# Kernel tuning notes

Measured on AMD Instinct MI355X. Metric: run time of the kernel, lower is better.

## Reference

```python
import jax, jax.numpy as jnp
import numpy as np

N, F, H, T, E, HOR = 50000, 24, 128, 12, 800000, 6


def setup_inputs() -> dict:
    key = jax.random.key(0)
    ks = jax.random.split(key, 16)
    x_seq = jax.random.normal(ks[0], (T, N, F), jnp.float32)
    ei_seq = jax.random.randint(ks[1], (T, 2, E), 0, N, jnp.int32)
    ea_seq = jax.random.uniform(ks[2], (T, E), jnp.float32)
    mask_seq = jax.random.bernoulli(ks[3], 0.9, (T, N))
    s = 1.0 / float(np.sqrt(H))
    def w(k, shape):
        return jax.random.uniform(k, shape, jnp.float32, -s, s)
    params = dict(
        Wz=w(ks[4], (F, H)), Wr=w(ks[5], (F, H)), Wh=w(ks[6], (F, H)),
        bz=jnp.zeros((H,), jnp.float32), br=jnp.zeros((H,), jnp.float32), bh=jnp.zeros((H,), jnp.float32),
        LWz=w(ks[7], (2 * H, H)), LWr=w(ks[8], (2 * H, H)), LWh=w(ks[9], (2 * H, H)),
        Lbz=w(ks[10], (H,)), Lbr=w(ks[11], (H,)), Lbh=w(ks[12], (H,)),
        headW=w(ks[13], (H, F)), headb=w(ks[14], (F,)),
    )
    return dict(x_seq=x_seq, ei_seq=ei_seq, ea_seq=ea_seq, mask_seq=mask_seq, id_seq=0, **params)


def _gcn(x, src, dst, ew, W, b):
    xw = x @ W                                                     # [N,H]
    deg = jnp.zeros((x.shape[0],), xw.dtype).at[dst].add(ew) + 1.0  # in-degree + self-loop
    dinv = jax.lax.rsqrt(deg)
    coef = dinv[src] * ew * dinv[dst]                              # [E]
    agg = jnp.zeros_like(xw).at[dst].add(xw[src] * coef[:, None])
    return agg + xw * (1.0 / deg)[:, None] + b                     # normalized self-loop term


def _cell(x, src, dst, ew, h, p):
    # TGCN (GCN-GRU) cell from pytorch_geometric_temporal
    z = jax.nn.sigmoid(jnp.concatenate([_gcn(x, src, dst, ew, p['Wz'], p['bz']), h], 1) @ p['LWz'] + p['Lbz'])
    r = jax.nn.sigmoid(jnp.concatenate([_gcn(x, src, dst, ew, p['Wr'], p['br']), h], 1) @ p['LWr'] + p['Lbr'])
    htil = jnp.tanh(jnp.concatenate([_gcn(x, src, dst, ew, p['Wh'], p['bh']), h * r], 1) @ p['LWh'] + p['Lbh'])
    return z * h + (1.0 - z) * htil


def _forward(x_seq, ei_seq, ea_seq, mask_seq, p):
    Nn, Hh = x_seq.shape[1], p['LWz'].shape[1]

    # Encoder over T steps: h_store keeps last hidden of every node ever present
    def enc(carry, inp):
        h_store, seen = carry
        x, ei, ew, mask = inp
        h_prev = jnp.where((mask & seen)[:, None], h_store, 0.0)
        h_new = _cell(x, ei[0], ei[1], ew, h_prev, p)
        return (jnp.where(mask[:, None], h_new, h_store), seen | mask), None

    init = (jnp.zeros((Nn, Hh), x_seq.dtype), jnp.zeros((Nn,), bool))
    (h_store, seen), _ = jax.lax.scan(enc, init, (x_seq, ei_seq, ea_seq, mask_seq))

    h_prev = jnp.where((mask_seq[-1] & seen)[:, None], h_store, 0.0)
    src_l, dst_l, ew_l = ei_seq[-1, 0], ei_seq[-1, 1], ea_seq[-1]

    def dec(carry, _):
        h, inp = carry
        h_new = _cell(inp, src_l, dst_l, ew_l, h, p)
        y = h_new @ p['headW'] + p['headb']
        return (h_new, y), y

    _, preds = jax.lax.scan(dec, (h_prev, x_seq[-1]), None, length=HOR)
    return preds  # [horizon, N, out_channels]


def reference(x_seq, ei_seq, ea_seq, mask_seq, id_seq, Wz, Wr, Wh, bz, br, bh,
              LWz, LWr, LWh, Lbz, Lbr, Lbh, headW, headb):
    p = dict(Wz=Wz, Wr=Wr, Wh=Wh, bz=bz, br=br, bh=bh,
             LWz=LWz, LWr=LWr, LWh=LWh, Lbz=Lbz, Lbr=Lbr, Lbh=Lbh,
             headW=headW, headb=headb)
    return _forward(x_seq, ei_seq, ea_seq, mask_seq, p)
```

## Files before the change

kernel.cpp:

```cpp
#include <hip/hip_runtime.h>

#define NN 50000
#define FF 24
#define HH 128
#define TT 12
#define EE 800000
#define HORZ 6


__global__ void k_maskdetect(const unsigned char* __restrict__ m, int* __restrict__ flag) {
    int i = blockIdx.x * 256 + threadIdx.x;
    if (i < 16384 && (i & 3) != 0 && m[i] != 0) atomicOr(flag, 1);
}

__global__ void k_maskconv(const unsigned char* __restrict__ mraw, const int* __restrict__ flag,
                           unsigned char* __restrict__ mout) {
    int i = blockIdx.x * 256 + threadIdx.x;
    if (i >= TT * NN) return;
    if (*flag) mout[i] = (mraw[i] != 0);
    else       mout[i] = (((const int*)mraw)[i] != 0);
}


__global__ void k_hist(const int* __restrict__ ei, int* __restrict__ cnt) {
    int idx = blockIdx.x * 256 + threadIdx.x;
    if (idx >= TT * EE) return;
    int t = idx / EE, e = idx - t * EE;
    int dst = ei[((size_t)t * 2 + 1) * EE + e];
    atomicAdd(&cnt[t * NN + dst], 1);
}

__global__ void k_scan(const int* __restrict__ cnt, int* __restrict__ offs,
                       int* __restrict__ cursor) {
    __shared__ int sums[1024];
    int t = blockIdx.x, tid = threadIdx.x;
    const int per = (NN + 1023) / 1024;
    int base = tid * per;
    int s = 0;
    for (int i = 0; i < per; i++) {
        int idx = base + i;
        if (idx < NN) s += cnt[t * NN + idx];
    }
    sums[tid] = s;
    __syncthreads();
    for (int off = 1; off < 1024; off <<= 1) {
        int tv = (tid >= off) ? sums[tid - off] : 0;
        __syncthreads();
        sums[tid] += tv;
        __syncthreads();
    }
    int run = sums[tid] - s;
    for (int i = 0; i < per; i++) {
        int idx = base + i;
        if (idx < NN) {
            offs[t * (NN + 1) + idx] = run;
            cursor[t * NN + idx] = run;
            run += cnt[t * NN + idx];
        }
    }
    if (tid == 1023) offs[t * (NN + 1) + NN] = sums[1023];
}

__global__ void k_fill(const int* __restrict__ ei, const float* __restrict__ ea,
                       int* __restrict__ cursor, int* __restrict__ srcs,
                       float* __restrict__ eav) {
    int idx = blockIdx.x * 256 + threadIdx.x;
    if (idx >= TT * EE) return;
    int t = idx / EE, e = idx - t * EE;
    int dst = ei[((size_t)t * 2 + 1) * EE + e];
    int src = ei[((size_t)t * 2 + 0) * EE + e];
    int pos = atomicAdd(&cursor[t * NN + dst], 1);
    srcs[(size_t)t * EE + pos] = src;
    eav[(size_t)t * EE + pos]  = ea[(size_t)t * EE + e];
}

__global__ void k_degdinv(const int* __restrict__ offs, const float* __restrict__ eav,
                          float* __restrict__ dinv) {
    int idx = blockIdx.x * 256 + threadIdx.x;
    if (idx >= TT * NN) return;
    int t = idx / NN, n = idx - t * NN;
    int b = offs[t * (NN + 1) + n], en = offs[t * (NN + 1) + n + 1];
    float s = 0.f;
    for (int j = b; j < en; j++) s += eav[(size_t)t * EE + j];
    dinv[idx] = rsqrtf(s + 1.0f);
}

__global__ void k_coef(const int* __restrict__ offs, const int* __restrict__ srcs,
                       const float* __restrict__ dinv, float* __restrict__ eav) {
    int idx = blockIdx.x * 256 + threadIdx.x;
    if (idx >= TT * NN) return;
    int t = idx / NN, n = idx - t * NN;
    int b = offs[t * (NN + 1) + n], en = offs[t * (NN + 1) + n + 1];
    float di = dinv[idx];
    for (int j = b; j < en; j++) {
        int s = srcs[(size_t)t * EE + j];
        eav[(size_t)t * EE + j] *= di * dinv[t * NN + s];
    }
}


__global__ void k_fold(const float* __restrict__ Wz, const float* __restrict__ Wr,
                       const float* __restrict__ Wh,
                       const float* __restrict__ bz, const float* __restrict__ br,
                       const float* __restrict__ bh,
                       const float* __restrict__ LWz, const float* __restrict__ LWr,
                       const float* __restrict__ LWh,
                       const float* __restrict__ Lbz, const float* __restrict__ Lbr,
                       const float* __restrict__ Lbh,
                       float* __restrict__ Call, float* __restrict__ b2) {
    int g = blockIdx.x, c = threadIdx.x;
    const float* W  = g == 0 ? Wz : (g == 1 ? Wr : Wh);
    const float* LW = g == 0 ? LWz : (g == 1 ? LWr : LWh);
    const float* bg = g == 0 ? bz : (g == 1 ? br : bh);
    const float* Lb = g == 0 ? Lbz : (g == 1 ? Lbr : Lbh);
    for (int j = 0; j < FF; j++) {
        float a = 0.f;
        for (int k = 0; k < HH; k++) a += W[j * HH + k] * LW[k * HH + c];
        Call[((size_t)g * FF + j) * HH + c] = a;
    }
    float a = Lb[c];
    for (int k = 0; k < HH; k++) a += bg[k] * LW[k * HH + c];
    b2[g * HH + c] = a;
}


__global__ void k_gather(const float* __restrict__ x, const int* __restrict__ offs,
                         const int* __restrict__ srcs, const float* __restrict__ eav,
                         const float* __restrict__ dinv, float* __restrict__ xe) {
    int idx = blockIdx.x * 256 + threadIdx.x;
    if (idx >= NN * FF) return;
    int n = idx / FF, f = idx - n * FF;
    int b = offs[n], en = offs[n + 1];
    float di = dinv[n];
    float acc = x[idx] * di * di;
    for (int j = b; j < en; j++) {
        acc += x[srcs[j] * FF + f] * eav[j];
    }
    xe[idx] = acc;
}


#define FMA8X(SARR, M0, K)                                                        \
    {                                                                             \
        float4 v_;                                                                \
        v_ = *(const float4*)&SARR[M0 + 0][K]; a0 += v_.x*w0 + v_.y*w1 + v_.z*w2 + v_.w*w3; \
        v_ = *(const float4*)&SARR[M0 + 1][K]; a1 += v_.x*w0 + v_.y*w1 + v_.z*w2 + v_.w*w3; \
        v_ = *(const float4*)&SARR[M0 + 2][K]; a2 += v_.x*w0 + v_.y*w1 + v_.z*w2 + v_.w*w3; \
        v_ = *(const float4*)&SARR[M0 + 3][K]; a3 += v_.x*w0 + v_.y*w1 + v_.z*w2 + v_.w*w3; \
        v_ = *(const float4*)&SARR[M0 + 4][K]; a4 += v_.x*w0 + v_.y*w1 + v_.z*w2 + v_.w*w3; \
        v_ = *(const float4*)&SARR[M0 + 5][K]; a5 += v_.x*w0 + v_.y*w1 + v_.z*w2 + v_.w*w3; \
        v_ = *(const float4*)&SARR[M0 + 6][K]; a6 += v_.x*w0 + v_.y*w1 + v_.z*w2 + v_.w*w3; \
        v_ = *(const float4*)&SARR[M0 + 7][K]; a7 += v_.x*w0 + v_.y*w1 + v_.z*w2 + v_.w*w3; \
    }

template <int DOHEAD>
__global__ __launch_bounds__(256) void k_cell(
        const float* __restrict__ xe, const float* __restrict__ hin,
        const unsigned char* __restrict__ gmask,
        const float* __restrict__ Call, const float* __restrict__ b2,
        const float* __restrict__ LWz, const float* __restrict__ LWr,
        const float* __restrict__ LWh,
        const unsigned char* __restrict__ wmask, float* __restrict__ hout,
        const float* __restrict__ headW, const float* __restrict__ headb,
        float* __restrict__ y) {
    __shared__ float s_xe[16][FF];
    __shared__ float s_h0[16][HH];
    __shared__ float s_z[16][HH];
    __shared__ float s_hr[16][HH];
    int nb = blockIdx.x * 16;
    int tid = threadIdx.x;

    for (int i = tid; i < 16 * FF; i += 256) {
        s_xe[i / FF][i % FF] = xe[(size_t)nb * FF + i];
    }
    for (int i = tid; i < 16 * HH; i += 256) {
        int m = i >> 7, k = i & 127;
        float v = hin[((size_t)nb + m) * HH + k];
        if (gmask && !gmask[nb + m]) v = 0.f;
        s_h0[m][k] = v;
    }
    __syncthreads();

    int g = tid >> 7, c = tid & 127;

    {
        const float* Cg   = Call + (size_t)g * FF * HH;
        const float* LWgb = (g ? LWr : LWz) + (size_t)HH * HH;
        float bb = b2[g * HH + c];
#pragma unroll
        for (int ch = 0; ch < 2; ch++) {
            int m0 = ch * 8;
            float a0 = bb, a1 = bb, a2 = bb, a3 = bb, a4 = bb, a5 = bb, a6 = bb, a7 = bb;
#pragma unroll
            for (int k = 0; k < FF; k += 4) {
                float w0 = Cg[(k + 0) * HH + c], w1 = Cg[(k + 1) * HH + c];
                float w2 = Cg[(k + 2) * HH + c], w3 = Cg[(k + 3) * HH + c];
                FMA8X(s_xe, m0, k);
            }
#pragma unroll 4
            for (int k = 0; k < HH; k += 4) {
                float w0 = LWgb[(k + 0) * HH + c], w1 = LWgb[(k + 1) * HH + c];
                float w2 = LWgb[(k + 2) * HH + c], w3 = LWgb[(k + 3) * HH + c];
                FMA8X(s_h0, m0, k);
            }
#pragma unroll
            for (int r = 0; r < 8; r++) {
                float a = (r == 0) ? a0 : (r == 1) ? a1 : (r == 2) ? a2 : (r == 3) ? a3
                        : (r == 4) ? a4 : (r == 5) ? a5 : (r == 6) ? a6 : a7;
                float s = 1.f / (1.f + __expf(-a));
                if (g == 0) s_z[m0 + r][c] = s;
                else        s_hr[m0 + r][c] = s * s_h0[m0 + r][c];
            }
        }
    }
    __syncthreads();

    {
        const float* Ch   = Call + (size_t)2 * FF * HH;
        const float* LWhb = LWh + (size_t)HH * HH;
        float bb = b2[2 * HH + c];
        int m0 = g * 8;
        float a0 = bb, a1 = bb, a2 = bb, a3 = bb, a4 = bb, a5 = bb, a6 = bb, a7 = bb;
#pragma unroll
        for (int k = 0; k < FF; k += 4) {
            float w0 = Ch[(k + 0) * HH + c], w1 = Ch[(k + 1) * HH + c];
            float w2 = Ch[(k + 2) * HH + c], w3 = Ch[(k + 3) * HH + c];
            FMA8X(s_xe, m0, k);
        }
#pragma unroll 4
        for (int k = 0; k < HH; k += 4) {
            float w0 = LWhb[(k + 0) * HH + c], w1 = LWhb[(k + 1) * HH + c];
            float w2 = LWhb[(k + 2) * HH + c], w3 = LWhb[(k + 3) * HH + c];
            FMA8X(s_hr, m0, k);
        }
#pragma unroll
        for (int r = 0; r < 8; r++) {
            float a = (r == 0) ? a0 : (r == 1) ? a1 : (r == 2) ? a2 : (r == 3) ? a3
                    : (r == 4) ? a4 : (r == 5) ? a5 : (r == 6) ? a6 : a7;
            int m = m0 + r;
            float e2 = __expf(2.f * a);
            float ht = 1.f - 2.f / (e2 + 1.f);
            float z = s_z[m][c];
            float h0v = s_h0[m][c];
            float hn = z * h0v + (1.f - z) * ht;
            int n = nb + m;
            if (wmask) {
                if (wmask[n]) hout[(size_t)n * HH + c] = hn;
            } else {
                hout[(size_t)n * HH + c] = hn;
            }
            if (DOHEAD) s_z[m][c] = hn;
        }
    }

    if (DOHEAD) {
        __syncthreads();
        for (int i = tid; i < 16 * FF; i += 256) {
            int m = i / FF, f = i - m * FF;
            float acc = headb[f];
#pragma unroll 8
            for (int cJ = 0; cJ < HH; cJ++) acc += s_z[m][cJ] * headW[cJ * FF + f];
            y[(size_t)nb * FF + i] = acc;
        }
    }
}

extern "C" void kernel_launch(void* const* d_in, const int* in_sizes, int n_in,
                              void* d_out, int out_size, void* d_ws, size_t ws_size,
                              hipStream_t stream) {
    const float* x_seq = (const float*)d_in[0];
    const int*   ei    = (const int*)d_in[1];
    const float* ea    = (const float*)d_in[2];
    const unsigned char* mraw = (const unsigned char*)d_in[3];
    const float* Wz  = (const float*)d_in[5];
    const float* Wr  = (const float*)d_in[6];
    const float* Wh  = (const float*)d_in[7];
    const float* bz  = (const float*)d_in[8];
    const float* br  = (const float*)d_in[9];
    const float* bh  = (const float*)d_in[10];
    const float* LWz = (const float*)d_in[11];
    const float* LWr = (const float*)d_in[12];
    const float* LWh = (const float*)d_in[13];
    const float* Lbz = (const float*)d_in[14];
    const float* Lbr = (const float*)d_in[15];
    const float* Lbh = (const float*)d_in[16];
    const float* headW = (const float*)d_in[17];
    const float* headb = (const float*)d_in[18];
    float* out = (float*)d_out;

    char* wp = (char*)d_ws;
    int*   cnt    = (int*)wp;   wp += sizeof(int) * TT * NN;
    int*   cursor = (int*)wp;   wp += sizeof(int) * TT * NN;
    int*   offs   = (int*)wp;   wp += sizeof(int) * TT * (NN + 1);
    int*   srcs   = (int*)wp;   wp += sizeof(int) * (size_t)TT * EE;
    float* eav    = (float*)wp; wp += sizeof(float) * (size_t)TT * EE;
    float* dinv   = (float*)wp; wp += sizeof(float) * TT * NN;
    float* hstore = (float*)wp; wp += sizeof(float) * (size_t)NN * HH;
    float* hp     = (float*)wp; wp += sizeof(float) * (size_t)NN * HH;
    float* xebuf  = (float*)wp; wp += sizeof(float) * NN * FF;
    float* Call   = (float*)wp; wp += sizeof(float) * 3 * FF * HH;
    float* b2     = (float*)wp; wp += sizeof(float) * 3 * HH;
    int*   mflag  = (int*)wp;   wp += 256;
    unsigned char* mask = (unsigned char*)wp; wp += TT * NN;
    if (ws_size < (size_t)(wp - (char*)d_ws)) return;

    hipMemsetAsync(mflag, 0, sizeof(int), stream);
    k_maskdetect<<<64, 256, 0, stream>>>(mraw, mflag);
    k_maskconv<<<(TT * NN + 255) / 256, 256, 0, stream>>>(mraw, mflag, mask);

    hipMemsetAsync(cnt, 0, sizeof(int) * TT * NN, stream);
    hipMemsetAsync(hstore, 0, sizeof(float) * NN * HH, stream);
    k_hist<<<(TT * EE + 255) / 256, 256, 0, stream>>>(ei, cnt);
    k_scan<<<TT, 1024, 0, stream>>>(cnt, offs, cursor);
    k_fill<<<(TT * EE + 255) / 256, 256, 0, stream>>>(ei, ea, cursor, srcs, eav);
    k_degdinv<<<(TT * NN + 255) / 256, 256, 0, stream>>>(offs, eav, dinv);
    k_coef<<<(TT * NN + 255) / 256, 256, 0, stream>>>(offs, srcs, dinv, eav);
    k_fold<<<3, 128, 0, stream>>>(Wz, Wr, Wh, bz, br, bh, LWz, LWr, LWh, Lbz, Lbr, Lbh, Call, b2);

    for (int t = 0; t < TT; t++) {
        const float* xt = x_seq + (size_t)t * NN * FF;
        const unsigned char* mt = mask + (size_t)t * NN;
        k_gather<<<(NN * FF + 255) / 256, 256, 0, stream>>>(
            xt, offs + t * (NN + 1), srcs + (size_t)t * EE, eav + (size_t)t * EE,
            dinv + t * NN, xebuf);
        k_cell<0><<<NN / 16, 256, 0, stream>>>(
            xebuf, hstore, mt, Call, b2, LWz, LWr, LWh, mt, hstore,
            nullptr, nullptr, nullptr);
    }

    const int*   offsl = offs + (TT - 1) * (NN + 1);
    const int*   srcsl = srcs + (size_t)(TT - 1) * EE;
    const float* eavl  = eav + (size_t)(TT - 1) * EE;
    const float* dil   = dinv + (TT - 1) * NN;
    for (int k = 0; k < HORZ; k++) {
        const float* xin = (k == 0) ? (x_seq + (size_t)(TT - 1) * NN * FF)
                                    : (out + (size_t)(k - 1) * NN * FF);
        k_gather<<<(NN * FF + 255) / 256, 256, 0, stream>>>(
            xin, offsl, srcsl, eavl, dil, xebuf);
        k_cell<1><<<NN / 16, 256, 0, stream>>>(
            xebuf, (k == 0) ? hstore : hp,
            (k == 0) ? (mask + (size_t)(TT - 1) * NN) : nullptr,
            Call, b2, LWz, LWr, LWh, nullptr, hp,
            headW, headb, out + (size_t)k * NN * FF);
    }
}
```

Before: 5.121 ms.

## Pack CSR edges into int2 and compute z and r gates together per thread

```diff
diff --git a/kernel.cpp b/kernel.cpp
--- a/kernel.cpp
+++ b/kernel.cpp
@@ -62,39 +62,38 @@
 }
 
 __global__ void k_fill(const int* __restrict__ ei, const float* __restrict__ ea,
-                       int* __restrict__ cursor, int* __restrict__ srcs,
-                       float* __restrict__ eav) {
+                       int* __restrict__ cursor, int2* __restrict__ edges) {
     int idx = blockIdx.x * 256 + threadIdx.x;
     if (idx >= TT * EE) return;
     int t = idx / EE, e = idx - t * EE;
     int dst = ei[((size_t)t * 2 + 1) * EE + e];
     int src = ei[((size_t)t * 2 + 0) * EE + e];
     int pos = atomicAdd(&cursor[t * NN + dst], 1);
-    srcs[(size_t)t * EE + pos] = src;
-    eav[(size_t)t * EE + pos]  = ea[(size_t)t * EE + e];
-}
-
-__global__ void k_degdinv(const int* __restrict__ offs, const float* __restrict__ eav,
+    edges[(size_t)t * EE + pos] = make_int2(src, __float_as_int(ea[(size_t)t * EE + e]));
+}
+
+__global__ void k_degdinv(const int* __restrict__ offs, const int2* __restrict__ edges,
                           float* __restrict__ dinv) {
     int idx = blockIdx.x * 256 + threadIdx.x;
     if (idx >= TT * NN) return;
     int t = idx / NN, n = idx - t * NN;
     int b = offs[t * (NN + 1) + n], en = offs[t * (NN + 1) + n + 1];
     float s = 0.f;
-    for (int j = b; j < en; j++) s += eav[(size_t)t * EE + j];
+    for (int j = b; j < en; j++) s += __int_as_float(edges[(size_t)t * EE + j].y);
     dinv[idx] = rsqrtf(s + 1.0f);
 }
 
-__global__ void k_coef(const int* __restrict__ offs, const int* __restrict__ srcs,
-                       const float* __restrict__ dinv, float* __restrict__ eav) {
+__global__ void k_coef(const int* __restrict__ offs, const float* __restrict__ dinv,
+                       int2* __restrict__ edges) {
     int idx = blockIdx.x * 256 + threadIdx.x;
     if (idx >= TT * NN) return;
     int t = idx / NN, n = idx - t * NN;
     int b = offs[t * (NN + 1) + n], en = offs[t * (NN + 1) + n + 1];
     float di = dinv[idx];
     for (int j = b; j < en; j++) {
-        int s = srcs[(size_t)t * EE + j];
-        eav[(size_t)t * EE + j] *= di * dinv[t * NN + s];
+        int2 p = edges[(size_t)t * EE + j];
+        float v = __int_as_float(p.y) * di * dinv[t * NN + p.x];
+        edges[(size_t)t * EE + j].y = __float_as_int(v);
     }
 }
 
@@ -125,7 +124,7 @@
 
 
 __global__ void k_gather(const float* __restrict__ x, const int* __restrict__ offs,
-                         const int* __restrict__ srcs, const float* __restrict__ eav,
+                         const int2* __restrict__ edges,
                          const float* __restrict__ dinv, float* __restrict__ xe) {
     int idx = blockIdx.x * 256 + threadIdx.x;
     if (idx >= NN * FF) return;
@@ -134,11 +133,41 @@
     float di = dinv[n];
     float acc = x[idx] * di * di;
     for (int j = b; j < en; j++) {
-        acc += x[srcs[j] * FF + f] * eav[j];
+        int2 p = edges[j];
+        acc += x[p.x * FF + f] * __int_as_float(p.y);
     }
     xe[idx] = acc;
 }
 
+
+#define FMA8X2(SARR, M0, K)                                                                  \
+    {                                                                                        \
+        float4 v_;                                                                           \
+        v_ = *(const float4*)&SARR[M0 + 0][K];                                               \
+        az0 += v_.x*wz0 + v_.y*wz1 + v_.z*wz2 + v_.w*wz3;                                    \
+        ar0 += v_.x*wr0 + v_.y*wr1 + v_.z*wr2 + v_.w*wr3;                                    \
+        v_ = *(const float4*)&SARR[M0 + 1][K];                                               \
+        az1 += v_.x*wz0 + v_.y*wz1 + v_.z*wz2 + v_.w*wz3;                                    \
+        ar1 += v_.x*wr0 + v_.y*wr1 + v_.z*wr2 + v_.w*wr3;                                    \
+        v_ = *(const float4*)&SARR[M0 + 2][K];                                               \
+        az2 += v_.x*wz0 + v_.y*wz1 + v_.z*wz2 + v_.w*wz3;                                    \
+        ar2 += v_.x*wr0 + v_.y*wr1 + v_.z*wr2 + v_.w*wr3;                                    \
+        v_ = *(const float4*)&SARR[M0 + 3][K];                                               \
+        az3 += v_.x*wz0 + v_.y*wz1 + v_.z*wz2 + v_.w*wz3;                                    \
+        ar3 += v_.x*wr0 + v_.y*wr1 + v_.z*wr2 + v_.w*wr3;                                    \
+        v_ = *(const float4*)&SARR[M0 + 4][K];                                               \
+        az4 += v_.x*wz0 + v_.y*wz1 + v_.z*wz2 + v_.w*wz3;                                    \
+        ar4 += v_.x*wr0 + v_.y*wr1 + v_.z*wr2 + v_.w*wr3;                                    \
+        v_ = *(const float4*)&SARR[M0 + 5][K];                                               \
+        az5 += v_.x*wz0 + v_.y*wz1 + v_.z*wz2 + v_.w*wz3;                                    \
+        ar5 += v_.x*wr0 + v_.y*wr1 + v_.z*wr2 + v_.w*wr3;                                    \
+        v_ = *(const float4*)&SARR[M0 + 6][K];                                               \
+        az6 += v_.x*wz0 + v_.y*wz1 + v_.z*wz2 + v_.w*wz3;                                    \
+        ar6 += v_.x*wr0 + v_.y*wr1 + v_.z*wr2 + v_.w*wr3;                                    \
+        v_ = *(const float4*)&SARR[M0 + 7][K];                                               \
+        az7 += v_.x*wz0 + v_.y*wz1 + v_.z*wz2 + v_.w*wz3;                                    \
+        ar7 += v_.x*wr0 + v_.y*wr1 + v_.z*wr2 + v_.w*wr3;                                    \
+    }
 
 #define FMA8X(SARR, M0, K)                                                        \
     {                                                                             \
@@ -182,35 +211,40 @@
     __syncthreads();
 
     int g = tid >> 7, c = tid & 127;
+    int m0 = g * 8;
 
     {
-        const float* Cg   = Call + (size_t)g * FF * HH;
-        const float* LWgb = (g ? LWr : LWz) + (size_t)HH * HH;
-        float bb = b2[g * HH + c];
+        const float* Cz   = Call;
+        const float* Cr   = Call + (size_t)FF * HH;
+        const float* LWzb = LWz + (size_t)HH * HH;
+        const float* LWrb = LWr + (size_t)HH * HH;
+        float bbz = b2[c], bbr = b2[HH + c];
+        float az0 = bbz, az1 = bbz, az2 = bbz, az3 = bbz, az4 = bbz, az5 = bbz, az6 = bbz, az7 = bbz;
+        float ar0 = bbr, ar1 = bbr, ar2 = bbr, ar3 = bbr, ar4 = bbr, ar5 = bbr, ar6 = bbr, ar7 = bbr;
 #pragma unroll
-        for (int ch = 0; ch < 2; ch++) {
-            int m0 = ch * 8;
-            float a0 = bb, a1 = bb, a2 = bb, a3 = bb, a4 = bb, a5 = bb, a6 = bb, a7 = bb;
+        for (int k = 0; k < FF; k += 4) {
+            float wz0 = Cz[(k + 0) * HH + c], wz1 = Cz[(k + 1) * HH + c];
+            float wz2 = Cz[(k + 2) * HH + c], wz3 = Cz[(k + 3) * HH + c];
+            float wr0 = Cr[(k + 0) * HH + c], wr1 = Cr[(k + 1) * HH + c];
+            float wr2 = Cr[(k + 2) * HH + c], wr3 = Cr[(k + 3) * HH + c];
+            FMA8X2(s_xe, m0, k);
+        }
+#pragma unroll 4
+        for (int k = 0; k < HH; k += 4) {
+            float wz0 = LWzb[(k + 0) * HH + c], wz1 = LWzb[(k + 1) * HH + c];
+            float wz2 = LWzb[(k + 2) * HH + c], wz3 = LWzb[(k + 3) * HH + c];
+            float wr0 = LWrb[(k + 0) * HH + c], wr1 = LWrb[(k + 1) * HH + c];
+            float wr2 = LWrb[(k + 2) * HH + c], wr3 = LWrb[(k + 3) * HH + c];
+            FMA8X2(s_h0, m0, k);
+        }
 #pragma unroll
-            for (int k = 0; k < FF; k += 4) {
-                float w0 = Cg[(k + 0) * HH + c], w1 = Cg[(k + 1) * HH + c];
-                float w2 = Cg[(k + 2) * HH + c], w3 = Cg[(k + 3) * HH + c];
-                FMA8X(s_xe, m0, k);
-            }
-#pragma unroll 4
-            for (int k = 0; k < HH; k += 4) {
-                float w0 = LWgb[(k + 0) * HH + c], w1 = LWgb[(k + 1) * HH + c];
-                float w2 = LWgb[(k + 2) * HH + c], w3 = LWgb[(k + 3) * HH + c];
-                FMA8X(s_h0, m0, k);
-            }
-#pragma unroll
-            for (int r = 0; r < 8; r++) {
-                float a = (r == 0) ? a0 : (r == 1) ? a1 : (r == 2) ? a2 : (r == 3) ? a3
-                        : (r == 4) ? a4 : (r == 5) ? a5 : (r == 6) ? a6 : a7;
-                float s = 1.f / (1.f + __expf(-a));
-                if (g == 0) s_z[m0 + r][c] = s;
-                else        s_hr[m0 + r][c] = s * s_h0[m0 + r][c];
-            }
+        for (int r = 0; r < 8; r++) {
+            float az = (r == 0) ? az0 : (r == 1) ? az1 : (r == 2) ? az2 : (r == 3) ? az3
+                     : (r == 4) ? az4 : (r == 5) ? az5 : (r == 6) ? az6 : az7;
+            float ar = (r == 0) ? ar0 : (r == 1) ? ar1 : (r == 2) ? ar2 : (r == 3) ? ar3
+                     : (r == 4) ? ar4 : (r == 5) ? ar5 : (r == 6) ? ar6 : ar7;
+            s_z[m0 + r][c]  = 1.f / (1.f + __expf(-az));
+            s_hr[m0 + r][c] = (1.f / (1.f + __expf(-ar))) * s_h0[m0 + r][c];
         }
     }
     __syncthreads();
@@ -219,7 +253,6 @@
         const float* Ch   = Call + (size_t)2 * FF * HH;
         const float* LWhb = LWh + (size_t)HH * HH;
         float bb = b2[2 * HH + c];
-        int m0 = g * 8;
         float a0 = bb, a1 = bb, a2 = bb, a3 = bb, a4 = bb, a5 = bb, a6 = bb, a7 = bb;
 #pragma unroll
         for (int k = 0; k < FF; k += 4) {
@@ -292,8 +325,7 @@
     int*   cnt    = (int*)wp;   wp += sizeof(int) * TT * NN;
     int*   cursor = (int*)wp;   wp += sizeof(int) * TT * NN;
     int*   offs   = (int*)wp;   wp += sizeof(int) * TT * (NN + 1);
-    int*   srcs   = (int*)wp;   wp += sizeof(int) * (size_t)TT * EE;
-    float* eav    = (float*)wp; wp += sizeof(float) * (size_t)TT * EE;
+    int2*  edges  = (int2*)wp;  wp += sizeof(int2) * (size_t)TT * EE;
     float* dinv   = (float*)wp; wp += sizeof(float) * TT * NN;
     float* hstore = (float*)wp; wp += sizeof(float) * (size_t)NN * HH;
     float* hp     = (float*)wp; wp += sizeof(float) * (size_t)NN * HH;
@@ -312,31 +344,29 @@
     hipMemsetAsync(hstore, 0, sizeof(float) * NN * HH, stream);
     k_hist<<<(TT * EE + 255) / 256, 256, 0, stream>>>(ei, cnt);
     k_scan<<<TT, 1024, 0, stream>>>(cnt, offs, cursor);
-    k_fill<<<(TT * EE + 255) / 256, 256, 0, stream>>>(ei, ea, cursor, srcs, eav);
-    k_degdinv<<<(TT * NN + 255) / 256, 256, 0, stream>>>(offs, eav, dinv);
-    k_coef<<<(TT * NN + 255) / 256, 256, 0, stream>>>(offs, srcs, dinv, eav);
+    k_fill<<<(TT * EE + 255) / 256, 256, 0, stream>>>(ei, ea, cursor, edges);
+    k_degdinv<<<(TT * NN + 255) / 256, 256, 0, stream>>>(offs, edges, dinv);
+    k_coef<<<(TT * NN + 255) / 256, 256, 0, stream>>>(offs, dinv, edges);
     k_fold<<<3, 128, 0, stream>>>(Wz, Wr, Wh, bz, br, bh, LWz, LWr, LWh, Lbz, Lbr, Lbh, Call, b2);
 
     for (int t = 0; t < TT; t++) {
         const float* xt = x_seq + (size_t)t * NN * FF;
         const unsigned char* mt = mask + (size_t)t * NN;
         k_gather<<<(NN * FF + 255) / 256, 256, 0, stream>>>(
-            xt, offs + t * (NN + 1), srcs + (size_t)t * EE, eav + (size_t)t * EE,
-            dinv + t * NN, xebuf);
+            xt, offs + t * (NN + 1), edges + (size_t)t * EE, dinv + t * NN, xebuf);
         k_cell<0><<<NN / 16, 256, 0, stream>>>(
             xebuf, hstore, mt, Call, b2, LWz, LWr, LWh, mt, hstore,
             nullptr, nullptr, nullptr);
     }
 
-    const int*   offsl = offs + (TT - 1) * (NN + 1);
-    const int*   srcsl = srcs + (size_t)(TT - 1) * EE;
-    const float* eavl  = eav + (size_t)(TT - 1) * EE;
+    const int*  offsl  = offs + (TT - 1) * (NN + 1);
+    const int2* edgesl = edges + (size_t)(TT - 1) * EE;
     const float* dil   = dinv + (TT - 1) * NN;
     for (int k = 0; k < HORZ; k++) {
         const float* xin = (k == 0) ? (x_seq + (size_t)(TT - 1) * NN * FF)
                                     : (out + (size_t)(k - 1) * NN * FF);
         k_gather<<<(NN * FF + 255) / 256, 256, 0, stream>>>(
-            xin, offsl, srcsl, eavl, dil, xebuf);
+            xin, offsl, edgesl, dil, xebuf);
         k_cell<1><<<NN / 16, 256, 0, stream>>>(
             xebuf, (k == 0) ? hstore : hp,
             (k == 0) ? (mask + (size_t)(TT - 1) * NN) : nullptr,
```

Result: no change. 5.121 ms (+0.0%).

## Fuse neighbor gather into GRU cell kernel and transpose weights for vector loads

Applied to the files above, without the earlier changes.

```diff
diff --git a/kernel.cpp b/kernel.cpp
--- a/kernel.cpp
+++ b/kernel.cpp
@@ -107,7 +107,9 @@
                        const float* __restrict__ LWh,
                        const float* __restrict__ Lbz, const float* __restrict__ Lbr,
                        const float* __restrict__ Lbh,
-                       float* __restrict__ Call, float* __restrict__ b2) {
+                       const float* __restrict__ headW,
+                       float* __restrict__ CallT, float* __restrict__ b2,
+                       float* __restrict__ LWT, float* __restrict__ headWT) {
     int g = blockIdx.x, c = threadIdx.x;
     const float* W  = g == 0 ? Wz : (g == 1 ? Wr : Wh);
     const float* LW = g == 0 ? LWz : (g == 1 ? LWr : LWh);
@@ -116,52 +118,75 @@
     for (int j = 0; j < FF; j++) {
         float a = 0.f;
         for (int k = 0; k < HH; k++) a += W[j * HH + k] * LW[k * HH + c];
-        Call[((size_t)g * FF + j) * HH + c] = a;
+        CallT[((size_t)g * HH + c) * FF + j] = a;
     }
     float a = Lb[c];
     for (int k = 0; k < HH; k++) a += bg[k] * LW[k * HH + c];
     b2[g * HH + c] = a;
-}
-
-
-__global__ void k_gather(const float* __restrict__ x, const int* __restrict__ offs,
-                         const int* __restrict__ srcs, const float* __restrict__ eav,
-                         const float* __restrict__ dinv, float* __restrict__ xe) {
-    int idx = blockIdx.x * 256 + threadIdx.x;
-    if (idx >= NN * FF) return;
-    int n = idx / FF, f = idx - n * FF;
-    int b = offs[n], en = offs[n + 1];
-    float di = dinv[n];
-    float acc = x[idx] * di * di;
-    for (int j = b; j < en; j++) {
-        acc += x[srcs[j] * FF + f] * eav[j];
-    }
-    xe[idx] = acc;
-}
-
-
-#define FMA8X(SARR, M0, K)                                                        \
-    {                                                                             \
-        float4 v_;                                                                \
-        v_ = *(const float4*)&SARR[M0 + 0][K]; a0 += v_.x*w0 + v_.y*w1 + v_.z*w2 + v_.w*w3; \
-        v_ = *(const float4*)&SARR[M0 + 1][K]; a1 += v_.x*w0 + v_.y*w1 + v_.z*w2 + v_.w*w3; \
-        v_ = *(const float4*)&SARR[M0 + 2][K]; a2 += v_.x*w0 + v_.y*w1 + v_.z*w2 + v_.w*w3; \
-        v_ = *(const float4*)&SARR[M0 + 3][K]; a3 += v_.x*w0 + v_.y*w1 + v_.z*w2 + v_.w*w3; \
-        v_ = *(const float4*)&SARR[M0 + 4][K]; a4 += v_.x*w0 + v_.y*w1 + v_.z*w2 + v_.w*w3; \
-        v_ = *(const float4*)&SARR[M0 + 5][K]; a5 += v_.x*w0 + v_.y*w1 + v_.z*w2 + v_.w*w3; \
-        v_ = *(const float4*)&SARR[M0 + 6][K]; a6 += v_.x*w0 + v_.y*w1 + v_.z*w2 + v_.w*w3; \
-        v_ = *(const float4*)&SARR[M0 + 7][K]; a7 += v_.x*w0 + v_.y*w1 + v_.z*w2 + v_.w*w3; \
+    for (int k = 0; k < HH; k++) {
+        LWT[((size_t)g * HH + c) * HH + k] = LW[(HH + k) * HH + c];
+    }
+    if (g == 0) {
+        for (int idx = c; idx < FF * HH; idx += 128) {
+            int f = idx / HH, cJ = idx - f * HH;
+            headWT[f * HH + cJ] = headW[cJ * FF + f];
+        }
+    }
+}
+
+
+#define FMA8X2(SARR, M0, K, WZ, WR)                                                          \
+    {                                                                                        \
+        float4 v_;                                                                           \
+        v_ = *(const float4*)&SARR[M0 + 0][K];                                               \
+        az0 += v_.x*WZ.x + v_.y*WZ.y + v_.z*WZ.z + v_.w*WZ.w;                                \
+        ar0 += v_.x*WR.x + v_.y*WR.y + v_.z*WR.z + v_.w*WR.w;                                \
+        v_ = *(const float4*)&SARR[M0 + 1][K];                                               \
+        az1 += v_.x*WZ.x + v_.y*WZ.y + v_.z*WZ.z + v_.w*WZ.w;                                \
+        ar1 += v_.x*WR.x + v_.y*WR.y + v_.z*WR.z + v_.w*WR.w;                                \
+        v_ = *(const float4*)&SARR[M0 + 2][K];                                               \
+        az2 += v_.x*WZ.x + v_.y*WZ.y + v_.z*WZ.z + v_.w*WZ.w;                                \
+        ar2 += v_.x*WR.x + v_.y*WR.y + v_.z*WR.z + v_.w*WR.w;                                \
+        v_ = *(const float4*)&SARR[M0 + 3][K];                                               \
+        az3 += v_.x*WZ.x + v_.y*WZ.y + v_.z*WZ.z + v_.w*WZ.w;                                \
+        ar3 += v_.x*WR.x + v_.y*WR.y + v_.z*WR.z + v_.w*WR.w;                                \
+        v_ = *(const float4*)&SARR[M0 + 4][K];                                               \
+        az4 += v_.x*WZ.x + v_.y*WZ.y + v_.z*WZ.z + v_.w*WZ.w;                                \
+        ar4 += v_.x*WR.x + v_.y*WR.y + v_.z*WR.z + v_.w*WR.w;                                \
+        v_ = *(const float4*)&SARR[M0 + 5][K];                                               \
+        az5 += v_.x*WZ.x + v_.y*WZ.y + v_.z*WZ.z + v_.w*WZ.w;                                \
+        ar5 += v_.x*WR.x + v_.y*WR.y + v_.z*WR.z + v_.w*WR.w;                                \
+        v_ = *(const float4*)&SARR[M0 + 6][K];                                               \
+        az6 += v_.x*WZ.x + v_.y*WZ.y + v_.z*WZ.z + v_.w*WZ.w;                                \
+        ar6 += v_.x*WR.x + v_.y*WR.y + v_.z*WR.z + v_.w*WR.w;                                \
+        v_ = *(const float4*)&SARR[M0 + 7][K];                                               \
+        az7 += v_.x*WZ.x + v_.y*WZ.y + v_.z*WZ.z + v_.w*WZ.w;                                \
+        ar7 += v_.x*WR.x + v_.y*WR.y + v_.z*WR.z + v_.w*WR.w;                                \
+    }
+
+#define FMA8X(SARR, M0, K, W4)                                                               \
+    {                                                                                        \
+        float4 v_;                                                                           \
+        v_ = *(const float4*)&SARR[M0 + 0][K]; a0 += v_.x*W4.x + v_.y*W4.y + v_.z*W4.z + v_.w*W4.w; \
+        v_ = *(const float4*)&SARR[M0 + 1][K]; a1 += v_.x*W4.x + v_.y*W4.y + v_.z*W4.z + v_.w*W4.w; \
+        v_ = *(const float4*)&SARR[M0 + 2][K]; a2 += v_.x*W4.x + v_.y*W4.y + v_.z*W4.z + v_.w*W4.w; \
+        v_ = *(const float4*)&SARR[M0 + 3][K]; a3 += v_.x*W4.x + v_.y*W4.y + v_.z*W4.z + v_.w*W4.w; \
+        v_ = *(const float4*)&SARR[M0 + 4][K]; a4 += v_.x*W4.x + v_.y*W4.y + v_.z*W4.z + v_.w*W4.w; \
+        v_ = *(const float4*)&SARR[M0 + 5][K]; a5 += v_.x*W4.x + v_.y*W4.y + v_.z*W4.z + v_.w*W4.w; \
+        v_ = *(const float4*)&SARR[M0 + 6][K]; a6 += v_.x*W4.x + v_.y*W4.y + v_.z*W4.z + v_.w*W4.w; \
+        v_ = *(const float4*)&SARR[M0 + 7][K]; a7 += v_.x*W4.x + v_.y*W4.y + v_.z*W4.z + v_.w*W4.w; \
     }
 
 template <int DOHEAD>
 __global__ __launch_bounds__(256) void k_cell(
-        const float* __restrict__ xe, const float* __restrict__ hin,
-        const unsigned char* __restrict__ gmask,
-        const float* __restrict__ Call, const float* __restrict__ b2,
-        const float* __restrict__ LWz, const float* __restrict__ LWr,
-        const float* __restrict__ LWh,
+        const float* __restrict__ x, const int* __restrict__ offs,
+        const int* __restrict__ srcs, const float* __restrict__ eav,
+        const float* __restrict__ dinv,
+        const float* __restrict__ hin, const unsigned char* __restrict__ gmask,
+        const float* __restrict__ CallT, const float* __restrict__ b2,
+        const float* __restrict__ LWT,
         const unsigned char* __restrict__ wmask, float* __restrict__ hout,
-        const float* __restrict__ headW, const float* __restrict__ headb,
+        const float* __restrict__ headWT, const float* __restrict__ headb,
         float* __restrict__ y) {
     __shared__ float s_xe[16][FF];
     __shared__ float s_h0[16][HH];
@@ -171,7 +196,15 @@
     int tid = threadIdx.x;
 
     for (int i = tid; i < 16 * FF; i += 256) {
-        s_xe[i / FF][i % FF] = xe[(size_t)nb * FF + i];
+        int m = i / FF, f = i - m * FF;
+        int n = nb + m;
+        int b = offs[n], en = offs[n + 1];
+        float di = dinv[n];
+        float acc = x[(size_t)n * FF + f] * di * di;
+        for (int j = b; j < en; j++) {
+            acc += x[(size_t)srcs[j] * FF + f] * eav[j];
+        }
+        s_xe[m][f] = acc;
     }
     for (int i = tid; i < 16 * HH; i += 256) {
         int m = i >> 7, k = i & 127;
@@ -182,56 +215,54 @@
     __syncthreads();
 
     int g = tid >> 7, c = tid & 127;
+    int m0 = g * 8;
 
     {
-        const float* Cg   = Call + (size_t)g * FF * HH;
-        const float* LWgb = (g ? LWr : LWz) + (size_t)HH * HH;
-        float bb = b2[g * HH + c];
+        const float* CzT  = CallT + (size_t)c * FF;
+        const float* CrT  = CallT + (size_t)(HH + c) * FF;
+        const float* LWzT = LWT + (size_t)c * HH;
+        const float* LWrT = LWT + (size_t)(HH + c) * HH;
+        float bbz = b2[c], bbr = b2[HH + c];
+        float az0 = bbz, az1 = bbz, az2 = bbz, az3 = bbz, az4 = bbz, az5 = bbz, az6 = bbz, az7 = bbz;
+        float ar0 = bbr, ar1 = bbr, ar2 = bbr, ar3 = bbr, ar4 = bbr, ar5 = bbr, ar6 = bbr, ar7 = bbr;
 #pragma unroll
-        for (int ch = 0; ch < 2; ch++) {
-            int m0 = ch * 8;
-            float a0 = bb, a1 = bb, a2 = bb, a3 = bb, a4 = bb, a5 = bb, a6 = bb, a7 = bb;
+        for (int k = 0; k < FF; k += 4) {
+            float4 wz = *(const float4*)&CzT[k];
+            float4 wr = *(const float4*)&CrT[k];
+            FMA8X2(s_xe, m0, k, wz, wr);
+        }
+#pragma unroll 4
+        for (int k = 0; k < HH; k += 4) {
+            float4 wz = *(const float4*)&LWzT[k];
+            float4 wr = *(const float4*)&LWrT[k];
+            FMA8X2(s_h0, m0, k, wz, wr);
+        }
 #pragma unroll
-            for (int k = 0; k < FF; k += 4) {
-                float w0 = Cg[(k + 0) * HH + c], w1 = Cg[(k + 1) * HH + c];
-                float w2 = Cg[(k + 2) * HH + c], w3 = Cg[(k + 3) * HH + c];
-                FMA8X(s_xe, m0, k);
-            }
-#pragma unroll 4
-            for (int k = 0; k < HH; k += 4) {
-                float w0 = LWgb[(k + 0) * HH + c], w1 = LWgb[(k + 1) * HH + c];
-                float w2 = LWgb[(k + 2) * HH + c], w3 = LWgb[(k + 3) * HH + c];
-                FMA8X(s_h0, m0, k);
-            }
-#pragma unroll
-            for (int r = 0; r < 8; r++) {
-                float a = (r == 0) ? a0 : (r == 1) ? a1 : (r == 2) ? a2 : (r == 3) ? a3
-                        : (r == 4) ? a4 : (r == 5) ? a5 : (r == 6) ? a6 : a7;
-                float s = 1.f / (1.f + __expf(-a));
-                if (g == 0) s_z[m0 + r][c] = s;
-                else        s_hr[m0 + r][c] = s * s_h0[m0 + r][c];
-            }
+        for (int r = 0; r < 8; r++) {
+            float az = (r == 0) ? az0 : (r == 1) ? az1 : (r == 2) ? az2 : (r == 3) ? az3
+                     : (r == 4) ? az4 : (r == 5) ? az5 : (r == 6) ? az6 : az7;
+            float ar = (r == 0) ? ar0 : (r == 1) ? ar1 : (r == 2) ? ar2 : (r == 3) ? ar3
+                     : (r == 4) ? ar4 : (r == 5) ? ar5 : (r == 6) ? ar6 : ar7;
+            s_z[m0 + r][c]  = 1.f / (1.f + __expf(-az));
+            s_hr[m0 + r][c] = (1.f / (1.f + __expf(-ar))) * s_h0[m0 + r][c];
         }
     }
     __syncthreads();
 
     {
-        const float* Ch   = Call + (size_t)2 * FF * HH;
-        const float* LWhb = LWh + (size_t)HH * HH;
+        const float* ChT  = CallT + (size_t)(2 * HH + c) * FF;
+        const float* LWhT = LWT + (size_t)(2 * HH + c) * HH;
         float bb = b2[2 * HH + c];
-        int m0 = g * 8;
         float a0 = bb, a1 = bb, a2 = bb, a3 = bb, a4 = bb, a5 = bb, a6 = bb, a7 = bb;
 #pragma unroll
         for (int k = 0; k < FF; k += 4) {
-            float w0 = Ch[(k + 0) * HH + c], w1 = Ch[(k + 1) * HH + c];
-            float w2 = Ch[(k + 2) * HH + c], w3 = Ch[(k + 3) * HH + c];
-            FMA8X(s_xe, m0, k);
+            float4 w4 = *(const float4*)&ChT[k];
+            FMA8X(s_xe, m0, k, w4);
         }
 #pragma unroll 4
         for (int k = 0; k < HH; k += 4) {
-            float w0 = LWhb[(k + 0) * HH + c], w1 = LWhb[(k + 1) * HH + c];
-            float w2 = LWhb[(k + 2) * HH + c], w3 = LWhb[(k + 3) * HH + c];
-            FMA8X(s_hr, m0, k);
+            float4 w4 = *(const float4*)&LWhT[k];
+            FMA8X(s_hr, m0, k, w4);
         }
 #pragma unroll
         for (int r = 0; r < 8; r++) {
@@ -257,9 +288,14 @@
         __syncthreads();
         for (int i = tid; i < 16 * FF; i += 256) {
             int m = i / FF, f = i - m * FF;
+            const float* hw = headWT + (size_t)f * HH;
             float acc = headb[f];
 #pragma unroll 8
-            for (int cJ = 0; cJ < HH; cJ++) acc += s_z[m][cJ] * headW[cJ * FF + f];
+            for (int cJ = 0; cJ < HH; cJ += 4) {
+                float4 hv = *(const float4*)&s_z[m][cJ];
+                float4 wv = *(const float4*)&hw[cJ];
+                acc += hv.x * wv.x + hv.y * wv.y + hv.z * wv.z + hv.w * wv.w;
+            }
             y[(size_t)nb * FF + i] = acc;
         }
     }
@@ -297,9 +333,10 @@
     float* dinv   = (float*)wp; wp += sizeof(float) * TT * NN;
     float* hstore = (float*)wp; wp += sizeof(float) * (size_t)NN * HH;
     float* hp     = (float*)wp; wp += sizeof(float) * (size_t)NN * HH;
-    float* xebuf  = (float*)wp; wp += sizeof(float) * NN * FF;
-    float* Call   = (float*)wp; wp += sizeof(float) * 3 * FF * HH;
+    float* CallT  = (float*)wp; wp += sizeof(float) * 3 * HH * FF;
     float* b2     = (float*)wp; wp += sizeof(float) * 3 * HH;
+    float* LWT    = (float*)wp; wp += sizeof(float) * 3 * HH * HH;
+    float* headWT = (float*)wp; wp += sizeof(float) * FF * HH;
     int*   mflag  = (int*)wp;   wp += 256;
     unsigned char* mask = (unsigned char*)wp; wp += TT * NN;
     if (ws_size < (size_t)(wp - (char*)d_ws)) return;
@@ -315,16 +352,15 @@
     k_fill<<<(TT * EE + 255) / 256, 256, 0, stream>>>(ei, ea, cursor, srcs, eav);
     k_degdinv<<<(TT * NN + 255) / 256, 256, 0, stream>>>(offs, eav, dinv);
     k_coef<<<(TT * NN + 255) / 256, 256, 0, stream>>>(offs, srcs, dinv, eav);
-    k_fold<<<3, 128, 0, stream>>>(Wz, Wr, Wh, bz, br, bh, LWz, LWr, LWh, Lbz, Lbr, Lbh, Call, b2);
+    k_fold<<<3, 128, 0, stream>>>(Wz, Wr, Wh, bz, br, bh, LWz, LWr, LWh, Lbz, Lbr, Lbh,
+                                  headW, CallT, b2, LWT, headWT);
 
     for (int t = 0; t < TT; t++) {
         const float* xt = x_seq + (size_t)t * NN * FF;
         const unsigned char* mt = mask + (size_t)t * NN;
-        k_gather<<<(NN * FF + 255) / 256, 256, 0, stream>>>(
+        k_cell<0><<<NN / 16, 256, 0, stream>>>(
             xt, offs + t * (NN + 1), srcs + (size_t)t * EE, eav + (size_t)t * EE,
-            dinv + t * NN, xebuf);
-        k_cell<0><<<NN / 16, 256, 0, stream>>>(
-            xebuf, hstore, mt, Call, b2, LWz, LWr, LWh, mt, hstore,
+            dinv + t * NN, hstore, mt, CallT, b2, LWT, mt, hstore,
             nullptr, nullptr, nullptr);
     }
 
@@ -335,12 +371,11 @@
     for (int k = 0; k < HORZ; k++) {
         const float* xin = (k == 0) ? (x_seq + (size_t)(TT - 1) * NN * FF)
                                     : (out + (size_t)(k - 1) * NN * FF);
-        k_gather<<<(NN * FF + 255) / 256, 256, 0, stream>>>(
-            xin, offsl, srcsl, eavl, dil, xebuf);
         k_cell<1><<<NN / 16, 256, 0, stream>>>(
-            xebuf, (k == 0) ? hstore : hp,
+            xin, offsl, srcsl, eavl, dil,
+            (k == 0) ? hstore : hp,
             (k == 0) ? (mask + (size_t)(TT - 1) * NN) : nullptr,
-            Call, b2, LWz, LWr, LWh, nullptr, hp,
-            headW, headb, out + (size_t)k * NN * FF);
-    }
-}
+            CallT, b2, LWT, nullptr, hp,
+            headWT, headb, out + (size_t)k * NN * FF);
+    }
+}
```

Result: slower. 6.529 ms (+27.5%).
